# Kernel tuning notes

Measured on AMD Instinct MI355X. Metric: run time of the kernel, lower is better.

The kernel has to match this reference:

```python
import jax, jax.numpy as jnp
import numpy as np

D = 1024
B, S = 4, 2048


def setup_inputs() -> dict:
    key = jax.random.key(0)
    ks = jax.random.split(key, 9)
    std = 1.0 / np.sqrt(D)
    x = jax.random.normal(ks[0], (B, S, D), dtype=jnp.float32)
    Wq = jax.random.normal(ks[1], (D, D), dtype=jnp.float32) * std
    bq = jax.random.normal(ks[2], (D,), dtype=jnp.float32) * std
    Wk = jax.random.normal(ks[3], (D, D), dtype=jnp.float32) * std
    bk = jax.random.normal(ks[4], (D,), dtype=jnp.float32) * std
    Wv = jax.random.normal(ks[5], (D, D), dtype=jnp.float32) * std
    bv = jax.random.normal(ks[6], (D,), dtype=jnp.float32) * std
    Wo = jax.random.normal(ks[7], (D, D), dtype=jnp.float32) * std
    bo = jax.random.normal(ks[8], (D,), dtype=jnp.float32) * std
    return {"x": x, "Wq": Wq, "bq": bq, "Wk": Wk, "bk": bk,
            "Wv": Wv, "bv": bv, "Wo": Wo, "bo": bo}


def reference(x, Wq, bq, Wk, bk, Wv, bv, Wo, bo):
    d = x.shape[-1]
    q = x @ Wq + bq          # [B, S, D]
    k = x @ Wk + bk          # [B, S, D] (first call: kv cache empty)
    v = x @ Wv + bv          # [B, S, D]
    scale = 1.0 / jnp.sqrt(jnp.asarray(d, dtype=x.dtype))
    att = jnp.einsum('bqd,bkd->bqk', q, k) * scale  # [B, S, S]
    sq, sk = q.shape[1], k.shape[1]
    causal = jnp.triu(jnp.ones((sq, sk), dtype=bool), k=1)
    att = jnp.where(causal, -jnp.inf, att)
    att = jax.nn.softmax(att, axis=-1)
    out = jnp.einsum('bqk,bkd->bqd', att, v)        # [B, S, D]
    return out @ Wo + bo
```

## Files before the change

kernel.cpp:

```cpp
#include <hip/hip_runtime.h>
#include <hip/hip_bf16.h>


typedef __attribute__((ext_vector_type(8))) __bf16 bf16x8;
typedef __attribute__((ext_vector_type(4))) float f32x4;
typedef __attribute__((ext_vector_type(8))) unsigned short u16x8;
typedef __attribute__((ext_vector_type(4))) float float4v;
typedef long long ll;

static __device__ __forceinline__ unsigned short f2b(float f) {
  unsigned int u = __float_as_uint(f);
  u += 0x7fffu + ((u >> 16) & 1u);
  return (unsigned short)(u >> 16);
}
static __device__ __forceinline__ float b2f(unsigned short b) {
  return __uint_as_float(((unsigned int)b) << 16);
}

static __device__ __forceinline__ void gload16(const unsigned short* g, unsigned short* l) {
  __builtin_amdgcn_global_load_lds(
      (const __attribute__((address_space(1))) void*)g,
      (__attribute__((address_space(3))) void*)l, 16, 0, 0);
}

__global__ __launch_bounds__(256) void cvt_f32_bf16(const float* __restrict__ in,
                                                    unsigned short* __restrict__ out,
                                                    long long n) {
  long long i = ((long long)blockIdx.x * 256 + threadIdx.x) * 8;
  if (i + 8 > n) return;
  float4v a = *(const float4v*)(in + i);
  float4v b = *(const float4v*)(in + i + 4);
  u16x8 o;
  o[0] = f2b(a[0]); o[1] = f2b(a[1]); o[2] = f2b(a[2]); o[3] = f2b(a[3]);
  o[4] = f2b(b[0]); o[5] = f2b(b[1]); o[6] = f2b(b[2]); o[7] = f2b(b[3]);
  *(u16x8*)(out + i) = o;
}

__global__ __launch_bounds__(256) void transpose_cvt(const float* __restrict__ in,
                                                     unsigned short* __restrict__ out, int n) {
  __shared__ float t[32][33];
  int bx = blockIdx.x * 32, by = blockIdx.y * 32;
  int tx = threadIdx.x, ty = threadIdx.y;
#pragma unroll
  for (int i = 0; i < 32; i += 8)
    t[ty + i][tx] = in[(ll)(by + ty + i) * n + bx + tx];
  __syncthreads();
#pragma unroll
  for (int i = 0; i < 32; i += 8)
    out[(ll)(bx + ty + i) * n + by + tx] = f2b(t[tx][ty + i]);
}

__global__ void concat2(const float* __restrict__ a, const float* __restrict__ b,
                        float* __restrict__ o, int n) {
  int i = blockIdx.x * 256 + threadIdx.x;
  if (i < n) { o[i] = a[i]; o[i + n] = b[i]; }
}

template <int CAUSAL>
__global__ __launch_bounds__(256, 2) void gemm_tn(
    const unsigned short* __restrict__ A, const unsigned short* __restrict__ B,
    const float* __restrict__ bias, void* __restrict__ C,
    int K, int lda, int ldb, int ldc,
    ll strideA, ll strideB, ll strideC,
    float alpha, int c_is_bf16, int bias_row) {
  if (CAUSAL == 1 && blockIdx.x > blockIdx.y) return;

  __shared__ unsigned short sA[2][128][64];
  __shared__ unsigned short sB[2][128][64];

  const int tid = threadIdx.x;
  const int w = tid >> 6, lane = tid & 63;
  const int bz = blockIdx.z;
  const unsigned short* Ab = A + (ll)bz * strideA;
  const unsigned short* Bb = B + (ll)bz * strideB;
  const int brow = blockIdx.y * 128, bcol = blockIdx.x * 128;
  const int wr = (w >> 1) * 64, wc = (w & 1) * 64;
  const int lr = lane & 15, lk = lane >> 4;

  const int Keff = (CAUSAL == 2) ? (brow + 128) : K;
  const int nt = Keff >> 6;

  f32x4 acc[4][4];
#pragma unroll
  for (int i = 0; i < 4; ++i)
#pragma unroll
    for (int n = 0; n < 4; ++n) acc[i][n] = (f32x4){0.f, 0.f, 0.f, 0.f};

  auto STAGE = [&](int buf, int kb) {
#pragma unroll
    for (int it = 0; it < 4; ++it) {
      const int chunk = it * 4 + w;
      const int slot = chunk * 64 + lane;
      const int row = slot >> 3;
      const int kg = (slot & 7) ^ (row & 7);
      gload16(Ab + (ll)(brow + row) * lda + kb + kg * 8, &sA[buf][0][0] + chunk * 512);
      gload16(Bb + (ll)(bcol + row) * ldb + kb + kg * 8, &sB[buf][0][0] + chunk * 512);
    }
  };

  auto COMPUTE = [&](int buf) {
#pragma unroll
    for (int kk = 0; kk < 64; kk += 32) {
      bf16x8 af[4], bfr[4];
      const int kgb = (kk >> 3) + lk;
      const int sw = (kgb ^ (lr & 7)) * 8;
#pragma unroll
      for (int i = 0; i < 4; ++i) af[i] = *(const bf16x8*)&sA[buf][wr + i * 16 + lr][sw];
#pragma unroll
      for (int n = 0; n < 4; ++n) bfr[n] = *(const bf16x8*)&sB[buf][wc + n * 16 + lr][sw];
#pragma unroll
      for (int i = 0; i < 4; ++i)
#pragma unroll
        for (int n = 0; n < 4; ++n)
          acc[i][n] = __builtin_amdgcn_mfma_f32_16x16x32_bf16(af[i], bfr[n], acc[i][n], 0, 0, 0);
    }
  };

  STAGE(0, 0);
  __syncthreads();
  int cur = 0;
  for (int t = 0; t < nt - 1; ++t) {
    STAGE(cur ^ 1, (t + 1) << 6);
    COMPUTE(cur);
    __syncthreads();
    cur ^= 1;
  }
  COMPUTE(cur);

  ll cbase = (ll)bz * strideC;
#pragma unroll
  for (int i = 0; i < 4; ++i) {
    int row = brow + wr + i * 16 + lk * 4;
#pragma unroll
    for (int n = 0; n < 4; ++n) {
      int col = bcol + wc + n * 16 + lr;
#pragma unroll
      for (int r = 0; r < 4; ++r) {
        float bvv = bias ? (bias_row ? bias[row + r] : bias[col]) : 0.0f;
        float v = (acc[i][n][r] + bvv) * alpha;
        ll idx = cbase + (ll)(row + r) * ldc + col;
        if (c_is_bf16) ((unsigned short*)C)[idx] = f2b(v);
        else ((float*)C)[idx] = v;
      }
    }
  }
}

__global__ __launch_bounds__(256) void softmax_row2048(unsigned short* __restrict__ S) {
  const int r = blockIdx.x, b = blockIdx.y;
  unsigned short* row = S + ((ll)b * 2048 + r) * 2048;
  const int tid = threadIdx.x;
  const int i0 = tid * 8;
  __shared__ float red[4];

  u16x8 v = *(const u16x8*)(row + i0);
  float f[8];
  float m = -3.0e38f;
#pragma unroll
  for (int j = 0; j < 8; ++j) {
    f[j] = (i0 + j <= r) ? b2f(v[j]) : -3.0e38f;
    m = fmaxf(m, f[j]);
  }
#pragma unroll
  for (int o = 1; o < 64; o <<= 1) m = fmaxf(m, __shfl_xor(m, o, 64));
  if ((tid & 63) == 0) red[tid >> 6] = m;
  __syncthreads();
  m = fmaxf(fmaxf(red[0], red[1]), fmaxf(red[2], red[3]));
  __syncthreads();

  float e[8];
  float s = 0.0f;
#pragma unroll
  for (int j = 0; j < 8; ++j) {
    e[j] = (i0 + j <= r) ? __expf(f[j] - m) : 0.0f;
    s += e[j];
  }
#pragma unroll
  for (int o = 1; o < 64; o <<= 1) s += __shfl_xor(s, o, 64);
  if ((tid & 63) == 0) red[tid >> 6] = s;
  __syncthreads();
  s = red[0] + red[1] + red[2] + red[3];
  float inv = 1.0f / s;
  u16x8 o8;
#pragma unroll
  for (int j = 0; j < 8; ++j) o8[j] = f2b(e[j] * inv);
  *(u16x8*)(row + i0) = o8;
}

extern "C" void kernel_launch(void* const* d_in, const int* in_sizes, int n_in,
                              void* d_out, int out_size, void* d_ws, size_t ws_size,
                              hipStream_t stream) {
  const float* x  = (const float*)d_in[0];
  const float* Wq = (const float*)d_in[1];
  const float* bq = (const float*)d_in[2];
  const float* Wk = (const float*)d_in[3];
  const float* bk = (const float*)d_in[4];
  const float* Wv = (const float*)d_in[5];
  const float* bv = (const float*)d_in[6];
  const float* Wo = (const float*)d_in[7];
  const float* bo = (const float*)d_in[8];

  const int B = 4, S = 2048, D = 1024;
  const ll MS = (ll)B * S;

  char* p = (char*)d_ws;
  unsigned short* xb   = (unsigned short*)p; p += MS * D * 2;
  unsigned short* Wqkt = (unsigned short*)p; p += (ll)2 * D * D * 2;
  unsigned short* Wvt  = (unsigned short*)p; p += (ll)D * D * 2;
  unsigned short* Wot  = (unsigned short*)p; p += (ll)D * D * 2;
  float*          bqkc = (float*)p;          p += 2 * D * 4;
  unsigned short* QKc  = (unsigned short*)p; p += MS * 2 * D * 2;
  unsigned short* Vt   = (unsigned short*)p; p += (ll)D * MS * 2;
  unsigned short* Sm   = (unsigned short*)p; p += (ll)B * S * S * 2;
  unsigned short* At   = (unsigned short*)p; p += MS * D * 2;

  dim3 blk(256);
  dim3 tblk(32, 8);

  cvt_f32_bf16<<<dim3(4096), blk, 0, stream>>>(x, xb, MS * D);
  transpose_cvt<<<dim3(32, 32), tblk, 0, stream>>>(Wq, Wqkt, D);
  transpose_cvt<<<dim3(32, 32), tblk, 0, stream>>>(Wk, Wqkt + (ll)D * D, D);
  transpose_cvt<<<dim3(32, 32), tblk, 0, stream>>>(Wv, Wvt, D);
  transpose_cvt<<<dim3(32, 32), tblk, 0, stream>>>(Wo, Wot, D);
  concat2<<<dim3(4), blk, 0, stream>>>(bq, bk, bqkc, D);

  gemm_tn<0><<<dim3(16, 64, 1), blk, 0, stream>>>(
      xb, Wqkt, bqkc, QKc, D, D, D, 2 * D, 0, 0, 0, 1.0f, 1, 0);

  gemm_tn<0><<<dim3(64, 8, 1), blk, 0, stream>>>(
      Wvt, xb, bv, Vt, D, D, D, (int)MS, 0, 0, 0, 1.0f, 1, 1);

  gemm_tn<1><<<dim3(16, 16, 4), blk, 0, stream>>>(
      QKc, QKc + D, nullptr, Sm, D, 2 * D, 2 * D, S,
      (ll)S * 2 * D, (ll)S * 2 * D, (ll)S * S, 0.03125f, 1, 0);

  softmax_row2048<<<dim3(S, B), blk, 0, stream>>>(Sm);

  gemm_tn<2><<<dim3(8, 16, 4), blk, 0, stream>>>(
      Sm, Vt, nullptr, At, S, S, (int)MS, D,
      (ll)S * S, (ll)S, (ll)S * D, 1.0f, 1, 0);

  gemm_tn<0><<<dim3(8, 64, 1), blk, 0, stream>>>(
      At, Wot, bo, d_out, D, D, D, D, 0, 0, 0, 1.0f, 0, 0);
}
```

Before: 360.3 us.

## Add 256x256 eight-wave GEMM with 4-stage LDS pipeline for QK projection and scores

Introduces a new GEMM kernel using 512 threads and 256x256 output tiles, with a four-buffer LDS ring, two-ahead global_load_lds prefetch interleaved with MFMA halves, explicit vmcnt waits, and s_setprio around MFMA blocks. It replaces the old 128x128 kernel for the fused Q/K projection and the causal QK^T score GEMM. The aim is more data reuse per tile and better overlap of loads with matrix math. The cost is coarser causal skipping (256-wide tiles compute more masked work), larger register and LDS use, and fewer blocks to fill the GPU.

Result: faster. 340.7 us (-5.4%).

```diff
diff --git a/kernel.cpp b/kernel.cpp
--- a/kernel.cpp
+++ b/kernel.cpp
@@ -63,8 +63,6 @@
     int K, int lda, int ldb, int ldc,
     ll strideA, ll strideB, ll strideC,
     float alpha, int c_is_bf16, int bias_row) {
-  if (CAUSAL == 1 && blockIdx.x > blockIdx.y) return;
-
   __shared__ unsigned short sA[2][128][64];
   __shared__ unsigned short sB[2][128][64];
 
@@ -139,6 +137,126 @@
         float bvv = bias ? (bias_row ? bias[row + r] : bias[col]) : 0.0f;
         float v = (acc[i][n][r] + bvv) * alpha;
         ll idx = cbase + (ll)(row + r) * ldc + col;
+        if (c_is_bf16) ((unsigned short*)C)[idx] = f2b(v);
+        else ((float*)C)[idx] = v;
+      }
+    }
+  }
+}
+
+template <int CAUSAL>
+__global__ __launch_bounds__(512, 2) void gemm8p(
+    const unsigned short* __restrict__ A, const unsigned short* __restrict__ B,
+    const float* __restrict__ bias, void* __restrict__ C,
+    int K, int lda, int ldb, int ldc,
+    ll strideA, ll strideB, ll strideC,
+    float alpha, int c_is_bf16) {
+  if (CAUSAL == 1 && blockIdx.x > blockIdx.y) return;
+
+  __shared__ unsigned short smem[4 * 16384];
+
+  const int tid = threadIdx.x;
+  const int wid = tid >> 6, lane = tid & 63;
+  const int wm = wid >> 2, wn = wid & 3;
+  const int lr = lane & 15, lk = lane >> 4;
+  const int bz = blockIdx.z;
+  const unsigned short* Ab = A + (ll)bz * strideA;
+  const unsigned short* Bb = B + (ll)bz * strideB;
+  const int brow = blockIdx.y * 256, bcol = blockIdx.x * 256;
+  const int nt = K >> 5;
+
+  f32x4 acc[8][4];
+#pragma unroll
+  for (int m = 0; m < 8; ++m)
+#pragma unroll
+    for (int n = 0; n < 4; ++n) acc[m][n] = (f32x4){0.f, 0.f, 0.f, 0.f};
+
+  auto STAGE_A = [&](int t) {
+    unsigned short* lds = &smem[0] + (t & 3) * 16384;
+    const int kb = t << 5;
+#pragma unroll
+    for (int h = 0; h < 2; ++h) {
+      const int c = wid * 2 + h;
+      const int row = c * 16 + (lane >> 2);
+      const int kg = (lane & 3) ^ ((row >> 1) & 3);
+      gload16(Ab + (ll)(brow + row) * lda + kb + kg * 8, lds + c * 512);
+    }
+  };
+  auto STAGE_B = [&](int t) {
+    unsigned short* lds = &smem[0] + (t & 3) * 16384 + 8192;
+    const int kb = t << 5;
+#pragma unroll
+    for (int h = 0; h < 2; ++h) {
+      const int c = wid * 2 + h;
+      const int row = c * 16 + (lane >> 2);
+      const int kg = (lane & 3) ^ ((row >> 1) & 3);
+      gload16(Bb + (ll)(bcol + row) * ldb + kb + kg * 8, lds + c * 512);
+    }
+  };
+
+  STAGE_A(0); STAGE_B(0);
+  STAGE_A(1); STAGE_B(1);
+
+  for (int t = 0; t < nt; ++t) {
+    if (t < nt - 1) asm volatile("s_waitcnt vmcnt(4)" ::: "memory");
+    else            asm volatile("s_waitcnt vmcnt(0)" ::: "memory");
+    __builtin_amdgcn_s_barrier();
+
+    const unsigned short* lds = &smem[0] + (t & 3) * 16384;
+    bf16x8 bfrag[4], afrag[4];
+
+#pragma unroll
+    for (int n = 0; n < 4; ++n) {
+      const int row = wn * 64 + n * 16 + lr;
+      const int slot = lk ^ ((row >> 1) & 3);
+      bfrag[n] = *(const bf16x8*)(lds + 8192 + row * 32 + slot * 8);
+    }
+#pragma unroll
+    for (int m = 0; m < 4; ++m) {
+      const int row = wm * 128 + m * 16 + lr;
+      const int slot = lk ^ ((row >> 1) & 3);
+      afrag[m] = *(const bf16x8*)(lds + row * 32 + slot * 8);
+    }
+    if (t + 2 < nt) STAGE_A(t + 2);
+    __builtin_amdgcn_s_barrier();
+    __builtin_amdgcn_s_setprio(1);
+#pragma unroll
+    for (int m = 0; m < 4; ++m)
+#pragma unroll
+      for (int n = 0; n < 4; ++n)
+        acc[m][n] = __builtin_amdgcn_mfma_f32_16x16x32_bf16(afrag[m], bfrag[n], acc[m][n], 0, 0, 0);
+    __builtin_amdgcn_s_setprio(0);
+    __builtin_amdgcn_s_barrier();
+
+#pragma unroll
+    for (int m = 0; m < 4; ++m) {
+      const int row = wm * 128 + (m + 4) * 16 + lr;
+      const int slot = lk ^ ((row >> 1) & 3);
+      afrag[m] = *(const bf16x8*)(lds + row * 32 + slot * 8);
+    }
+    if (t + 2 < nt) STAGE_B(t + 2);
+    __builtin_amdgcn_s_barrier();
+    __builtin_amdgcn_s_setprio(1);
+#pragma unroll
+    for (int m = 0; m < 4; ++m)
+#pragma unroll
+      for (int n = 0; n < 4; ++n)
+        acc[m + 4][n] = __builtin_amdgcn_mfma_f32_16x16x32_bf16(afrag[m], bfrag[n], acc[m + 4][n], 0, 0, 0);
+    __builtin_amdgcn_s_setprio(0);
+  }
+
+  ll cbase = (ll)bz * strideC;
+#pragma unroll
+  for (int m = 0; m < 8; ++m) {
+    const int row0 = brow + wm * 128 + m * 16 + lk * 4;
+#pragma unroll
+    for (int n = 0; n < 4; ++n) {
+      const int col = bcol + wn * 64 + n * 16 + lr;
+#pragma unroll
+      for (int r = 0; r < 4; ++r) {
+        float bvv = bias ? bias[col] : 0.0f;
+        float v = (acc[m][n][r] + bvv) * alpha;
+        ll idx = cbase + (ll)(row0 + r) * ldc + col;
         if (c_is_bf16) ((unsigned short*)C)[idx] = f2b(v);
         else ((float*)C)[idx] = v;
       }
@@ -215,6 +333,7 @@
   unsigned short* At   = (unsigned short*)p; p += MS * D * 2;
 
   dim3 blk(256);
+  dim3 blk512(512);
   dim3 tblk(32, 8);
 
   cvt_f32_bf16<<<dim3(4096), blk, 0, stream>>>(x, xb, MS * D);
@@ -224,15 +343,15 @@
   transpose_cvt<<<dim3(32, 32), tblk, 0, stream>>>(Wo, Wot, D);
   concat2<<<dim3(4), blk, 0, stream>>>(bq, bk, bqkc, D);
 
-  gemm_tn<0><<<dim3(16, 64, 1), blk, 0, stream>>>(
-      xb, Wqkt, bqkc, QKc, D, D, D, 2 * D, 0, 0, 0, 1.0f, 1, 0);
+  gemm8p<0><<<dim3(8, 32, 1), blk512, 0, stream>>>(
+      xb, Wqkt, bqkc, QKc, D, D, D, 2 * D, 0, 0, 0, 1.0f, 1);
 
   gemm_tn<0><<<dim3(64, 8, 1), blk, 0, stream>>>(
       Wvt, xb, bv, Vt, D, D, D, (int)MS, 0, 0, 0, 1.0f, 1, 1);
 
-  gemm_tn<1><<<dim3(16, 16, 4), blk, 0, stream>>>(
+  gemm8p<1><<<dim3(8, 8, 4), blk512, 0, stream>>>(
       QKc, QKc + D, nullptr, Sm, D, 2 * D, 2 * D, S,
-      (ll)S * 2 * D, (ll)S * 2 * D, (ll)S * S, 0.03125f, 1, 0);
+      (ll)S * 2 * D, (ll)S * 2 * D, (ll)S * S, 0.03125f, 1);
 
   softmax_row2048<<<dim3(S, B), blk, 0, stream>>>(Sm);
 
```
